# Optimization experiments

Hardware: AMD Instinct MI355X
Metric: run time of the kernel (lower is better)

Reference implementation:

```python
import jax, jax.numpy as jnp
import numpy as np

HIDDEN = 64
EMBED = 16
N_AGENTS = 1024
TRACK_LEN = 8


def setup_inputs() -> dict:
    key = jax.random.key(0)
    ks = jax.random.split(key, 6)
    s = lambda fan_in: 1.0 / np.sqrt(fan_in)
    return {
        "hidden_state": jax.random.normal(ks[0], (1, N_AGENTS, HIDDEN), jnp.float32),
        "group_track": jax.random.normal(ks[1], (N_AGENTS, TRACK_LEN, 2), jnp.float32),
        "W_e": jax.random.normal(ks[2], (2, EMBED), jnp.float32) * s(2),
        "b_e": jnp.zeros((EMBED,), jnp.float32),
        "W1": jax.random.normal(ks[3], (EMBED + HIDDEN, 2 * HIDDEN), jnp.float32) * s(EMBED + HIDDEN),
        "b1": jnp.zeros((2 * HIDDEN,), jnp.float32),
        "W2": jax.random.normal(ks[4], (2 * HIDDEN, HIDDEN), jnp.float32) * s(2 * HIDDEN),
        "b2": jnp.zeros((HIDDEN,), jnp.float32),
    }


def reference(hidden_state, group_track, W_e, b_e, W1, b1, W2, b2):
    n = group_track.shape[0]
    ends = group_track[:, -1, :]                       # [N, 2] end positions
    # rel[c, j] = end_j - end_c  (relative neighbor end pos per center agent)
    rel = ends[None, :, :] - ends[:, None, :]          # [N, N, 2]
    emb = rel @ W_e + b_e                              # [N, N, E]
    h = jnp.broadcast_to(hidden_state[0][None, :, :], (n, n, hidden_state.shape[-1]))
    x = jnp.concatenate([h, emb], axis=-1)             # [N, N, E+H] (hidden first, as in torch)
    y = jax.nn.relu(x @ W1 + b1)                       # [N, N, 2H]
    z = jax.nn.relu(y @ W2 + b2)                       # [N, N, H]
    pooled = z.max(axis=1)                             # max over neighbors -> [N, H]
    return pooled[None]                                # [1, N, H]
```

## Files before the change

kernel.cpp:

```cpp
#include <hip/hip_runtime.h>


#define N_AG 1024
#define JT 2

typedef __attribute__((ext_vector_type(8))) _Float16 half8;
typedef __attribute__((ext_vector_type(4))) float floatx4;
typedef __attribute__((ext_vector_type(4))) unsigned int uintx4;

__device__ __forceinline__ unsigned short f2h(float f) {
  return __builtin_bit_cast(unsigned short, (_Float16)f);
}

__device__ __forceinline__ unsigned pk_sub_relu(unsigned a, unsigned u) {
  unsigned d;
  asm("v_pk_add_f16 %0, %1, %2 neg_lo:[0,1] neg_hi:[0,1]\n\t"
      "v_pk_max_f16 %0, %0, 0"
      : "=v"(d) : "v"(a), "v"(u));
  return d;
}

__global__ __launch_bounds__(128) void prep_all(
    const float* __restrict__ hidden,
    const float* __restrict__ track,
    const float* __restrict__ We,
    const float* __restrict__ be,
    const float* __restrict__ W1,
    const float* __restrict__ b1,
    const float* __restrict__ W2,
    unsigned short* __restrict__ Ah,
    float* __restrict__ M2f,
    unsigned short* __restrict__ W2T)
{
  const int jb = blockIdx.x;
  const int j0 = jb * JT;
  const int k  = threadIdx.x;
  __shared__ float hs[JT][64];
  hs[k >> 6][k & 63] = hidden[j0 * 64 + k];
  __syncthreads();

  float m20 = 0.f, m21 = 0.f, cb = b1[k];
#pragma unroll
  for (int t = 0; t < 16; ++t) {
    float w1v = W1[(64 + t) * 128 + k];
    m20 += We[t] * w1v;
    m21 += We[16 + t] * w1v;
    cb  += be[t] * w1v;
  }
  float acc[JT];
#pragma unroll
  for (int jj = 0; jj < JT; ++jj) {
    float e0 = track[(j0 + jj) * 16 + 14];
    float e1 = track[(j0 + jj) * 16 + 15];
    acc[jj] = e0 * m20 + e1 * m21 + cb;
  }
#pragma unroll 8
  for (int t = 0; t < 64; ++t) {
    float w = W1[t * 128 + k];
#pragma unroll
    for (int jj = 0; jj < JT; ++jj) acc[jj] += hs[jj][t] * w;
  }
#pragma unroll
  for (int jj = 0; jj < JT; ++jj)
    __builtin_nontemporal_store(f2h(acc[jj]), &Ah[(j0 + jj) * 128 + k]);

  if (jb == 0) {
    M2f[k]       = m20;
    M2f[128 + k] = m21;
  }
  if (jb < 32) {
#pragma unroll
    for (int q = 0; q < 2; ++q) {
      int idx = jb * 256 + q * 128 + k;
      int n = idx >> 7, c = idx & 127;
      W2T[n * 128 + c] = f2h(W2[c * 64 + n]);
    }
  }
}

__global__ __launch_bounds__(256, 2) void pool_main(
    const unsigned short* __restrict__ Ah,
    const float* __restrict__ M2f,
    const float* __restrict__ track,
    const unsigned short* __restrict__ W2T,
    const float* __restrict__ b2,
    float* __restrict__ out)
{
  const int i0   = blockIdx.x * 2;
  const int lane = threadIdx.x & 63;
  const int w    = threadIdx.x >> 6;
  const int m    = lane & 15;
  const int quad = lane >> 4;

  const int TSTEP = 4 * 16 * 128;
  const unsigned short* base = Ah + (w * 16 + m) * 128 + quad * 8;

  uintx4 buf0[4], buf1[4];
#pragma unroll
  for (int kk = 0; kk < 4; ++kk) buf0[kk] = *(const uintx4*)(base + kk * 32);
#pragma unroll
  for (int kk = 0; kk < 4; ++kk) buf1[kk] = *(const uintx4*)(base + TSTEP + kk * 32);

  const float a0 = track[i0 * 16 + 14];
  const float a1 = track[i0 * 16 + 15];
  const float c0 = track[(i0 + 1) * 16 + 14];
  const float c1 = track[(i0 + 1) * 16 + 15];
  unsigned upkA[4][4], upkB[4][4];
#pragma unroll
  for (int kk = 0; kk < 4; ++kk) {
#pragma unroll
    for (int p = 0; p < 4; ++p) {
      int k0 = kk * 32 + quad * 8 + 2 * p;
      float m0 = M2f[k0],     m0h = M2f[128 + k0];
      float m1 = M2f[k0 + 1], m1h = M2f[128 + k0 + 1];
      upkA[kk][p] = (unsigned)f2h(a0 * m0 + a1 * m0h) | ((unsigned)f2h(a0 * m1 + a1 * m1h) << 16);
      upkB[kk][p] = (unsigned)f2h(c0 * m0 + c1 * m0h) | ((unsigned)f2h(c0 * m1 + c1 * m1h) << 16);
    }
  }

  half8 bfrag[4][4];
#pragma unroll
  for (int nt = 0; nt < 4; ++nt)
#pragma unroll
    for (int kk = 0; kk < 4; ++kk)
      bfrag[nt][kk] = *(const half8*)(W2T + (nt * 16 + m) * 128 + kk * 32 + quad * 8);

  floatx4 mxA[4], mxB[4];
#pragma unroll
  for (int nt = 0; nt < 4; ++nt) {
    mxA[nt] = (floatx4){-3e38f, -3e38f, -3e38f, -3e38f};
    mxB[nt] = (floatx4){-3e38f, -3e38f, -3e38f, -3e38f};
  }

  const unsigned short* pn = base + 2 * TSTEP;

  auto body = [&](uintx4 (&BUF)[4], bool do_load) {
    uintx4 au[4];
#pragma unroll
    for (int kk = 0; kk < 4; ++kk)
#pragma unroll
      for (int p = 0; p < 4; ++p) au[kk][p] = pk_sub_relu(BUF[kk][p], upkA[kk][p]);
    __builtin_amdgcn_s_setprio(1);
#pragma unroll
    for (int nt = 0; nt < 4; ++nt) {
      floatx4 acc = (floatx4){0.f, 0.f, 0.f, 0.f};
#pragma unroll
      for (int kk = 0; kk < 4; ++kk)
        acc = __builtin_amdgcn_mfma_f32_16x16x32_f16(
            __builtin_bit_cast(half8, au[kk]), bfrag[nt][kk], acc, 0, 0, 0);
#pragma unroll
      for (int r = 0; r < 4; ++r) mxA[nt][r] = fmaxf(mxA[nt][r], acc[r]);
    }
    __builtin_amdgcn_s_setprio(0);
#pragma unroll
    for (int kk = 0; kk < 4; ++kk)
#pragma unroll
      for (int p = 0; p < 4; ++p) au[kk][p] = pk_sub_relu(BUF[kk][p], upkB[kk][p]);
    if (do_load) {
#pragma unroll
      for (int kk = 0; kk < 4; ++kk) BUF[kk] = *(const uintx4*)(pn + kk * 32);
      pn += TSTEP;
    }
    __builtin_amdgcn_s_setprio(1);
#pragma unroll
    for (int nt = 0; nt < 4; ++nt) {
      floatx4 acc = (floatx4){0.f, 0.f, 0.f, 0.f};
#pragma unroll
      for (int kk = 0; kk < 4; ++kk)
        acc = __builtin_amdgcn_mfma_f32_16x16x32_f16(
            __builtin_bit_cast(half8, au[kk]), bfrag[nt][kk], acc, 0, 0, 0);
#pragma unroll
      for (int r = 0; r < 4; ++r) mxB[nt][r] = fmaxf(mxB[nt][r], acc[r]);
    }
    __builtin_amdgcn_s_setprio(0);
  };

#pragma unroll 1
  for (int t2 = 0; t2 < 14; t2 += 2) {
    body(buf0, true);
    body(buf1, true);
  }
  body(buf0, false);
  body(buf1, false);

  __shared__ float red[2][4][64];
#pragma unroll
  for (int nt = 0; nt < 4; ++nt) {
    float a = fmaxf(fmaxf(mxA[nt][0], mxA[nt][1]), fmaxf(mxA[nt][2], mxA[nt][3]));
    a = fmaxf(a, __shfl_xor(a, 16, 64));
    a = fmaxf(a, __shfl_xor(a, 32, 64));
    float b = fmaxf(fmaxf(mxB[nt][0], mxB[nt][1]), fmaxf(mxB[nt][2], mxB[nt][3]));
    b = fmaxf(b, __shfl_xor(b, 16, 64));
    b = fmaxf(b, __shfl_xor(b, 32, 64));
    if (quad == 0) {
      red[0][w][nt * 16 + m] = a;
      red[1][w][nt * 16 + m] = b;
    }
  }
  __syncthreads();
  if (threadIdx.x < 128) {
    int g = threadIdx.x >> 6, n = threadIdx.x & 63;
    float v = fmaxf(fmaxf(red[g][0][n], red[g][1][n]), fmaxf(red[g][2][n], red[g][3][n]));
    v += b2[n];
    out[(i0 + g) * 64 + n] = v > 0.f ? v : 0.f;
  }
}

extern "C" void kernel_launch(void* const* d_in, const int* in_sizes, int n_in,
                              void* d_out, int out_size, void* d_ws, size_t ws_size,
                              hipStream_t stream) {
  const float* hidden = (const float*)d_in[0];
  const float* track  = (const float*)d_in[1];
  const float* We     = (const float*)d_in[2];
  const float* be     = (const float*)d_in[3];
  const float* W1     = (const float*)d_in[4];
  const float* b1     = (const float*)d_in[5];
  const float* W2     = (const float*)d_in[6];
  const float* b2     = (const float*)d_in[7];
  float* out = (float*)d_out;

  char* ws = (char*)d_ws;
  unsigned short* Ah  = (unsigned short*)ws;
  float*          M2f = (float*)(ws + 262144);
  unsigned short* W2T = (unsigned short*)(ws + 263168);

  prep_all<<<N_AG / JT, 128, 0, stream>>>(hidden, track, We, be, W1, b1, W2, Ah, M2f, W2T);
  pool_main<<<N_AG / 2, 256, 0, stream>>>(Ah, M2f, track, W2T, b2, out);
}
```

Before: 93.02 us.

## Fuse prep and pooling kernels with a grid-wide atomic barrier

Merges the prep kernel and the pooling kernel into one persistent launch. Blocks first compute their slice of the projected hidden table, then wait at a global atomic-counter barrier before pooling. W2 is now transposed into shared memory by every block and M2 is kept in LDS, which removes the separate workspace buffers. The setprio hints are also dropped. This trades a kernel launch and an inter-kernel gap for a memset, redundant per-block W2 transposition, and a spin barrier that relies on all 512 blocks being co-resident.

Measured after the change: 135.5 us. 1.46x slower.

```diff
diff --git a/kernel.cpp b/kernel.cpp
--- a/kernel.cpp
+++ b/kernel.cpp
@@ -2,7 +2,6 @@
 
 
 #define N_AG 1024
-#define JT 2
 
 typedef __attribute__((ext_vector_type(8))) _Float16 half8;
 typedef __attribute__((ext_vector_type(4))) float floatx4;
@@ -20,7 +19,7 @@
   return d;
 }
 
-__global__ __launch_bounds__(128) void prep_all(
+__global__ __launch_bounds__(256, 2) void fused(
     const float* __restrict__ hidden,
     const float* __restrict__ track,
     const float* __restrict__ We,
@@ -28,67 +27,61 @@
     const float* __restrict__ W1,
     const float* __restrict__ b1,
     const float* __restrict__ W2,
+    const float* __restrict__ b2,
     unsigned short* __restrict__ Ah,
-    float* __restrict__ M2f,
-    unsigned short* __restrict__ W2T)
-{
-  const int jb = blockIdx.x;
-  const int j0 = jb * JT;
-  const int k  = threadIdx.x;
-  __shared__ float hs[JT][64];
-  hs[k >> 6][k & 63] = hidden[j0 * 64 + k];
-  __syncthreads();
-
-  float m20 = 0.f, m21 = 0.f, cb = b1[k];
-#pragma unroll
-  for (int t = 0; t < 16; ++t) {
-    float w1v = W1[(64 + t) * 128 + k];
-    m20 += We[t] * w1v;
-    m21 += We[16 + t] * w1v;
-    cb  += be[t] * w1v;
-  }
-  float acc[JT];
-#pragma unroll
-  for (int jj = 0; jj < JT; ++jj) {
-    float e0 = track[(j0 + jj) * 16 + 14];
-    float e1 = track[(j0 + jj) * 16 + 15];
-    acc[jj] = e0 * m20 + e1 * m21 + cb;
-  }
-#pragma unroll 8
-  for (int t = 0; t < 64; ++t) {
-    float w = W1[t * 128 + k];
-#pragma unroll
-    for (int jj = 0; jj < JT; ++jj) acc[jj] += hs[jj][t] * w;
-  }
-#pragma unroll
-  for (int jj = 0; jj < JT; ++jj)
-    __builtin_nontemporal_store(f2h(acc[jj]), &Ah[(j0 + jj) * 128 + k]);
-
-  if (jb == 0) {
-    M2f[k]       = m20;
-    M2f[128 + k] = m21;
-  }
-  if (jb < 32) {
-#pragma unroll
-    for (int q = 0; q < 2; ++q) {
-      int idx = jb * 256 + q * 128 + k;
-      int n = idx >> 7, c = idx & 127;
-      W2T[n * 128 + c] = f2h(W2[c * 64 + n]);
-    }
-  }
-}
-
-__global__ __launch_bounds__(256, 2) void pool_main(
-    const unsigned short* __restrict__ Ah,
-    const float* __restrict__ M2f,
-    const float* __restrict__ track,
-    const unsigned short* __restrict__ W2T,
-    const float* __restrict__ b2,
+    unsigned int* __restrict__ done,
     float* __restrict__ out)
 {
-  const int i0   = blockIdx.x * 2;
-  const int lane = threadIdx.x & 63;
-  const int w    = threadIdx.x >> 6;
+  const int b   = blockIdx.x;
+  const int tid = threadIdx.x;
+
+  __shared__ float hs[2][64];
+  __shared__ float M2l[2][128];
+  __shared__ __align__(16) unsigned short W2T[64][128];
+  __shared__ float red[2][4][64];
+
+  if (tid < 128) hs[tid >> 6][tid & 63] = hidden[b * 128 + tid];
+#pragma unroll 8
+  for (int q = tid; q < 64 * 128; q += 256) {
+    int n = q >> 7, c = q & 127;
+    W2T[n][c] = f2h(W2[c * 64 + n]);
+  }
+  __syncthreads();
+
+  {
+    const int col = tid & 127;
+    const int row = tid >> 7;
+    float m20 = 0.f, m21 = 0.f, cb = b1[col];
+#pragma unroll
+    for (int t = 0; t < 16; ++t) {
+      float w1v = W1[(64 + t) * 128 + col];
+      m20 += We[t] * w1v;
+      m21 += We[16 + t] * w1v;
+      cb  += be[t] * w1v;
+    }
+    const int j = b * 2 + row;
+    const float e0 = track[j * 16 + 14];
+    const float e1 = track[j * 16 + 15];
+    float acc = e0 * m20 + e1 * m21 + cb;
+#pragma unroll 8
+    for (int t = 0; t < 64; ++t) acc += hs[row][t] * W1[t * 128 + col];
+    Ah[j * 128 + col] = f2h(acc);
+    if (row == 0) { M2l[0][col] = m20; M2l[1][col] = m21; }
+  }
+
+  __syncthreads();
+  if (tid == 0) {
+    __threadfence();
+    __hip_atomic_fetch_add(done, 1u, __ATOMIC_ACQ_REL, __HIP_MEMORY_SCOPE_AGENT);
+    while (__hip_atomic_load(done, __ATOMIC_ACQUIRE, __HIP_MEMORY_SCOPE_AGENT) < 512u)
+      __builtin_amdgcn_s_sleep(2);
+    __threadfence();
+  }
+  __syncthreads();
+
+  const int i0   = b * 2;
+  const int lane = tid & 63;
+  const int w    = tid >> 6;
   const int m    = lane & 15;
   const int quad = lane >> 4;
 
@@ -111,8 +104,8 @@
 #pragma unroll
     for (int p = 0; p < 4; ++p) {
       int k0 = kk * 32 + quad * 8 + 2 * p;
-      float m0 = M2f[k0],     m0h = M2f[128 + k0];
-      float m1 = M2f[k0 + 1], m1h = M2f[128 + k0 + 1];
+      float m0 = M2l[0][k0],     m0h = M2l[1][k0];
+      float m1 = M2l[0][k0 + 1], m1h = M2l[1][k0 + 1];
       upkA[kk][p] = (unsigned)f2h(a0 * m0 + a1 * m0h) | ((unsigned)f2h(a0 * m1 + a1 * m1h) << 16);
       upkB[kk][p] = (unsigned)f2h(c0 * m0 + c1 * m0h) | ((unsigned)f2h(c0 * m1 + c1 * m1h) << 16);
     }
@@ -123,7 +116,7 @@
   for (int nt = 0; nt < 4; ++nt)
 #pragma unroll
     for (int kk = 0; kk < 4; ++kk)
-      bfrag[nt][kk] = *(const half8*)(W2T + (nt * 16 + m) * 128 + kk * 32 + quad * 8);
+      bfrag[nt][kk] = *(const half8*)&W2T[nt * 16 + m][kk * 32 + quad * 8];
 
   floatx4 mxA[4], mxB[4];
 #pragma unroll
@@ -140,7 +133,6 @@
     for (int kk = 0; kk < 4; ++kk)
 #pragma unroll
       for (int p = 0; p < 4; ++p) au[kk][p] = pk_sub_relu(BUF[kk][p], upkA[kk][p]);
-    __builtin_amdgcn_s_setprio(1);
 #pragma unroll
     for (int nt = 0; nt < 4; ++nt) {
       floatx4 acc = (floatx4){0.f, 0.f, 0.f, 0.f};
@@ -151,7 +143,6 @@
 #pragma unroll
       for (int r = 0; r < 4; ++r) mxA[nt][r] = fmaxf(mxA[nt][r], acc[r]);
     }
-    __builtin_amdgcn_s_setprio(0);
 #pragma unroll
     for (int kk = 0; kk < 4; ++kk)
 #pragma unroll
@@ -161,7 +152,6 @@
       for (int kk = 0; kk < 4; ++kk) BUF[kk] = *(const uintx4*)(pn + kk * 32);
       pn += TSTEP;
     }
-    __builtin_amdgcn_s_setprio(1);
 #pragma unroll
     for (int nt = 0; nt < 4; ++nt) {
       floatx4 acc = (floatx4){0.f, 0.f, 0.f, 0.f};
@@ -172,7 +162,6 @@
 #pragma unroll
       for (int r = 0; r < 4; ++r) mxB[nt][r] = fmaxf(mxB[nt][r], acc[r]);
     }
-    __builtin_amdgcn_s_setprio(0);
   };
 
 #pragma unroll 1
@@ -183,23 +172,22 @@
   body(buf0, false);
   body(buf1, false);
 
-  __shared__ float red[2][4][64];
 #pragma unroll
   for (int nt = 0; nt < 4; ++nt) {
     float a = fmaxf(fmaxf(mxA[nt][0], mxA[nt][1]), fmaxf(mxA[nt][2], mxA[nt][3]));
     a = fmaxf(a, __shfl_xor(a, 16, 64));
     a = fmaxf(a, __shfl_xor(a, 32, 64));
-    float b = fmaxf(fmaxf(mxB[nt][0], mxB[nt][1]), fmaxf(mxB[nt][2], mxB[nt][3]));
-    b = fmaxf(b, __shfl_xor(b, 16, 64));
-    b = fmaxf(b, __shfl_xor(b, 32, 64));
+    float bb = fmaxf(fmaxf(mxB[nt][0], mxB[nt][1]), fmaxf(mxB[nt][2], mxB[nt][3]));
+    bb = fmaxf(bb, __shfl_xor(bb, 16, 64));
+    bb = fmaxf(bb, __shfl_xor(bb, 32, 64));
     if (quad == 0) {
       red[0][w][nt * 16 + m] = a;
-      red[1][w][nt * 16 + m] = b;
-    }
-  }
-  __syncthreads();
-  if (threadIdx.x < 128) {
-    int g = threadIdx.x >> 6, n = threadIdx.x & 63;
+      red[1][w][nt * 16 + m] = bb;
+    }
+  }
+  __syncthreads();
+  if (tid < 128) {
+    int g = tid >> 6, n = tid & 63;
     float v = fmaxf(fmaxf(red[g][0][n], red[g][1][n]), fmaxf(red[g][2][n], red[g][3][n]));
     v += b2[n];
     out[(i0 + g) * 64 + n] = v > 0.f ? v : 0.f;
@@ -220,10 +208,9 @@
   float* out = (float*)d_out;
 
   char* ws = (char*)d_ws;
-  unsigned short* Ah  = (unsigned short*)ws;
-  float*          M2f = (float*)(ws + 262144);
-  unsigned short* W2T = (unsigned short*)(ws + 263168);
-
-  prep_all<<<N_AG / JT, 128, 0, stream>>>(hidden, track, We, be, W1, b1, W2, Ah, M2f, W2T);
-  pool_main<<<N_AG / 2, 256, 0, stream>>>(Ah, M2f, track, W2T, b2, out);
-}
+  unsigned short* Ah   = (unsigned short*)ws;
+  unsigned int*   done = (unsigned int*)(ws + 262144);
+
+  hipMemsetAsync(done, 0, 4, stream);
+  fused<<<N_AG / 2, 256, 0, stream>>>(hidden, track, We, be, W1, b1, W2, b2, Ah, done, out);
+}
```
